# Optimization experiments

Hardware: AMD Instinct MI355X
Metric: run time of the kernel (lower is better)

Reference implementation:

```python
import jax, jax.numpy as jnp
import numpy as np

B, M = 2, 4096
N1, N2, N3 = 16384, 8192, 4096
OFFSET = (0.0, -40.0, -3.0)
LR_VS = (0.4, 0.4, 1.0)
HR1_VS = (0.05, 0.05, 0.1)
HR2_VS = (0.1, 0.1, 0.2)
HR3_VS = (0.2, 0.2, 0.4)
RADIUS = 1.0
NS1, NS2, NS3 = 128, 32, 16
BN_EPS = 1e-3


def _rand_idx(key, n, dims):
    kz, ky, kx = jax.random.split(key, 3)
    z = jax.random.randint(kz, (B, n, 1), 0, dims[0], dtype=jnp.int32)
    y = jax.random.randint(ky, (B, n, 1), 0, dims[1], dtype=jnp.int32)
    x = jax.random.randint(kx, (B, n, 1), 0, dims[2], dtype=jnp.int32)
    return jnp.concatenate([z, y, x], axis=-1)


def setup_inputs() -> dict:
    key = jax.random.key(0)
    ks = jax.random.split(key, 16)
    s = 0.1
    inp = {}
    # voxel indices are (z, y, x) per the original coors layout
    inp["lr_idx"] = _rand_idx(ks[0], M, (5, 200, 176))
    inp["hr1_idx"] = _rand_idx(ks[1], N1, (40, 1600, 1408))
    inp["hr2_idx"] = _rand_idx(ks[2], N2, (20, 800, 704))
    inp["hr3_idx"] = _rand_idx(ks[3], N3, (10, 400, 352))
    inp["lr_feat"] = jax.random.normal(ks[4], (B, M, 64), jnp.float32)
    inp["hr1_feat"] = jax.random.normal(ks[5], (B, N1, 16), jnp.float32)
    inp["hr2_feat"] = jax.random.normal(ks[6], (B, N2, 32), jnp.float32)
    inp["hr3_feat"] = jax.random.normal(ks[7], (B, N3, 64), jnp.float32)
    # Grouper shared-MLP weights (single layer each; +3 channels for use_xyz)
    inp["w14"] = jax.random.normal(ks[8], (19, 32), jnp.float32) * s
    inp["b14"] = jnp.zeros((32,), jnp.float32)
    inp["w24"] = jax.random.normal(ks[9], (35, 32), jnp.float32) * s
    inp["b24"] = jnp.zeros((32,), jnp.float32)
    inp["w34"] = jax.random.normal(ks[10], (67, 32), jnp.float32) * s
    inp["b34"] = jnp.zeros((32,), jnp.float32)
    # conv4_out: 1x1x1 sparse conv == dense matmul per voxel, then BN + ReLU
    inp["w_out"] = jax.random.normal(ks[11], (160, 64), jnp.float32) * s
    inp["bn_gamma"] = jnp.ones((64,), jnp.float32)
    inp["bn_beta"] = jnp.zeros((64,), jnp.float32)
    inp["bn_mean"] = jnp.zeros((64,), jnp.float32)
    inp["bn_var"] = jnp.ones((64,), jnp.float32)
    return inp


def idx_to_xyz(idx, vs):
    # indices are (z,y,x); original does indices[:, [3,2,1]] * voxel_size + offset + 0.5*voxel_size
    vs = jnp.asarray(vs, jnp.float32)
    off = jnp.asarray(OFFSET, jnp.float32)
    return idx[..., ::-1].astype(jnp.float32) * vs + off + 0.5 * vs


def ball_query(lr_xyz, hr_xyz, nsample):
    # first-nsample-within-radius semantics of pointnet2 ball_query
    d2 = jnp.sum((lr_xyz[:, None, :] - hr_xyz[None, :, :]) ** 2, axis=-1)  # [M, N]
    n = hr_xyz.shape[0]
    cand = jnp.where(d2 < RADIUS * RADIUS, jnp.arange(n, dtype=jnp.int32), n)
    neg, _ = jax.lax.top_k(-cand, nsample)  # smallest nsample candidate indices
    idx = -neg
    idx = jnp.where(idx == n, idx[:, :1], idx)  # pad with first valid neighbor
    return jnp.where(idx == n, 0, idx)          # no neighbor at all -> index 0


def group_pool(lr_xyz, hr_xyz, hr_feat, nsample, w, b):
    idx = ball_query(lr_xyz, hr_xyz, nsample)          # [M, ns]
    g_xyz = hr_xyz[idx] - lr_xyz[:, None, :]           # [M, ns, 3] relative coords
    g = jnp.concatenate([g_xyz, hr_feat[idx]], axis=-1)  # [M, ns, 3+C]
    h = jax.nn.relu(jnp.einsum('msc,co->mso', g, w) + b)
    return h.max(axis=1)                                # [M, Cout] max-pool over neighbors


def reference(lr_idx, hr1_idx, hr2_idx, hr3_idx, lr_feat, hr1_feat, hr2_feat, hr3_feat,
              w14, b14, w24, b24, w34, b34, w_out, bn_gamma, bn_beta, bn_mean, bn_var):
    lr_xyz = idx_to_xyz(lr_idx, LR_VS)                  # [B, M, 3]
    f14 = jax.vmap(lambda l, h, f: group_pool(l, h, f, NS1, w14, b14))(lr_xyz, idx_to_xyz(hr1_idx, HR1_VS), hr1_feat)
    f24 = jax.vmap(lambda l, h, f: group_pool(l, h, f, NS2, w24, b24))(lr_xyz, idx_to_xyz(hr2_idx, HR2_VS), hr2_feat)
    f34 = jax.vmap(lambda l, h, f: group_pool(l, h, f, NS3, w34, b34))(lr_xyz, idx_to_xyz(hr3_idx, HR3_VS), hr3_feat)
    cat = jnp.concatenate([lr_feat, f14, f24, f34], axis=-1)  # [B, M, 160] (in-place feature growth)
    y = jnp.einsum('bmc,co->bmo', cat, w_out)
    y = (y - bn_mean) * jax.lax.rsqrt(bn_var + BN_EPS) * bn_gamma + bn_beta
    return jax.nn.relu(y)
```

## Files before the change

### kernel.cpp

```cpp
#include <hip/hip_runtime.h>

#define BM   8192
#define NN1  16384
#define NN2  8192
#define NN3  4096
#define NB   80
#define NBLK 32
#define CHUNK 2048
#define TSZ  768
#define QCAP 512

#define OFF_LRS   0
#define OFF_S1    32768
#define OFF_S2    163840
#define OFF_S3    229376
#define OFF_F1    262144
#define OFF_F2    1310720
#define OFF_F3    1835008
#define OFF_PART  2097152
#define OFF_START 2117632
#define OFF_WP    2118656
#define OFF_SHIFT 2128896
#define WS_FLOATS 2128960


__global__ __launch_bounds__(256) void kprep(
    const int* __restrict__ lr_idx, const int* __restrict__ h1i,
    const int* __restrict__ h2i, const int* __restrict__ h3i,
    const float* __restrict__ f1, const float* __restrict__ f2, const float* __restrict__ f3,
    const float* __restrict__ w14, const float* __restrict__ b14,
    const float* __restrict__ w24, const float* __restrict__ b24,
    const float* __restrict__ w34, const float* __restrict__ b34,
    const float* __restrict__ wout, const float* __restrict__ gam,
    const float* __restrict__ bet, const float* __restrict__ mean,
    const float* __restrict__ var, float* __restrict__ ws)
{
    __shared__ int hist[640];
    int bx = blockIdx.x, tid = threadIdx.x;

    if (bx < NBLK) {
        for (int e = tid; e < 640; e += 256) hist[e] = 0;
        __syncthreads();
        int base_it = bx * CHUNK;
        for (int t = tid; t < CHUNK; t += 256) {
            int e = base_it + t;
            int T, iy; float vsx;
            if (e < 8192)            { T = 6 + (e>>12); iy = lr_idx[e*3+1]; vsx = 0.4f; }
            else { int r = e - 8192;
              if (r < 32768)         { int b = r>>14; T = b;   iy = h1i[r*3+1]; vsx = 0.05f; }
              else { r -= 32768;
                if (r < 16384)       { int b = r>>13; T = 2+b; iy = h2i[r*3+1]; vsx = 0.1f; }
                else { r -= 16384; int b = r>>12; T = 4+b; iy = h3i[r*3+1]; vsx = 0.2f; }
              }
            }
            float y = __fadd_rn(__fadd_rn(__fmul_rn((float)iy, vsx), -40.0f), __fmul_rn(0.5f, vsx));
            int k = min(NB-1, max(0, (int)floorf(y + 40.0f)));
            atomicAdd(&hist[T*80 + k], 1);
        }
        __syncthreads();
        for (int e = tid; e < 640; e += 256)
            reinterpret_cast<int*>(ws)[OFF_PART + bx*640 + e] = hist[e];
        return;
    }

    int e = (bx - NBLK) * 256 + tid;

    if (e < 262144) {
        int o2 = e & 7, jj = e >> 3;
        const float4* fv = reinterpret_cast<const float4*>(f1) + jj*4;
        const float4* w4 = reinterpret_cast<const float4*>(w14);
        float4 acc = reinterpret_cast<const float4*>(b14)[o2];
        float fr[16];
        #pragma unroll
        for (int c4 = 0; c4 < 4; ++c4) {
            float4 f = fv[c4];
            fr[c4*4] = f.x; fr[c4*4+1] = f.y; fr[c4*4+2] = f.z; fr[c4*4+3] = f.w;
        }
        #pragma unroll
        for (int c = 0; c < 16; ++c) {
            float4 w = w4[(3+c)*8 + o2];
            acc.x = fmaf(fr[c], w.x, acc.x); acc.y = fmaf(fr[c], w.y, acc.y);
            acc.z = fmaf(fr[c], w.z, acc.z); acc.w = fmaf(fr[c], w.w, acc.w);
        }
        reinterpret_cast<float4*>(ws + OFF_F1)[jj*8 + o2] = acc;
        return;
    }
    e -= 262144;
    if (e < 131072) {
        int o2 = e & 7, jj = e >> 3;
        const float4* fv = reinterpret_cast<const float4*>(f2) + jj*8;
        const float4* w4 = reinterpret_cast<const float4*>(w24);
        float4 acc = reinterpret_cast<const float4*>(b24)[o2];
        #pragma unroll
        for (int cc = 0; cc < 32; cc += 16) {
            float fr[16];
            #pragma unroll
            for (int c4 = 0; c4 < 4; ++c4) {
                float4 f = fv[cc/4 + c4];
                fr[c4*4] = f.x; fr[c4*4+1] = f.y; fr[c4*4+2] = f.z; fr[c4*4+3] = f.w;
            }
            #pragma unroll
            for (int c = 0; c < 16; ++c) {
                float4 w = w4[(3+cc+c)*8 + o2];
                acc.x = fmaf(fr[c], w.x, acc.x); acc.y = fmaf(fr[c], w.y, acc.y);
                acc.z = fmaf(fr[c], w.z, acc.z); acc.w = fmaf(fr[c], w.w, acc.w);
            }
        }
        reinterpret_cast<float4*>(ws + OFF_F2)[jj*8 + o2] = acc;
        return;
    }
    e -= 131072;
    if (e < 65536) {
        int o2 = e & 7, jj = e >> 3;
        const float4* fv = reinterpret_cast<const float4*>(f3) + jj*16;
        const float4* w4 = reinterpret_cast<const float4*>(w34);
        float4 acc = reinterpret_cast<const float4*>(b34)[o2];
        #pragma unroll
        for (int cc = 0; cc < 64; cc += 16) {
            float fr[16];
            #pragma unroll
            for (int c4 = 0; c4 < 4; ++c4) {
                float4 f = fv[cc/4 + c4];
                fr[c4*4] = f.x; fr[c4*4+1] = f.y; fr[c4*4+2] = f.z; fr[c4*4+3] = f.w;
            }
            #pragma unroll
            for (int c = 0; c < 16; ++c) {
                float4 w = w4[(3+cc+c)*8 + o2];
                acc.x = fmaf(fr[c], w.x, acc.x); acc.y = fmaf(fr[c], w.y, acc.y);
                acc.z = fmaf(fr[c], w.z, acc.z); acc.w = fmaf(fr[c], w.w, acc.w);
            }
        }
        reinterpret_cast<float4*>(ws + OFF_F3)[jj*8 + o2] = acc;
        return;
    }
    e -= 65536;

    if (e < 10240) {
        int o = e & 63;
        float sc = gam[o] * (1.0f / sqrtf(var[o] + 1e-3f));
        ws[OFF_WP + e] = wout[e] * sc;
    } else if (e < 10304) {
        int o = e - 10240;
        float sc = gam[o] * (1.0f / sqrtf(var[o] + 1e-3f));
        ws[OFF_SHIFT + o] = bet[o] - mean[o] * sc;
    }
}

__global__ __launch_bounds__(1024) void ksort(
    const int* __restrict__ lr_idx, const int* __restrict__ h1i,
    const int* __restrict__ h2i, const int* __restrict__ h3i,
    float* __restrict__ ws)
{
    __shared__ int totS[640];
    __shared__ int stt[648];
    __shared__ int cur[640];
    int t = threadIdx.x, bx = blockIdx.x;
    int* wsi = reinterpret_cast<int*>(ws);

    int tot = 0, mypre = 0;
    if (t < 640) {
        #pragma unroll
        for (int b = 0; b < NBLK; ++b) {
            int p = wsi[OFF_PART + b*640 + t];
            tot += p;
            if (b < bx) mypre += p;
        }
        totS[t] = tot;
    }
    __syncthreads();
    int wid = t >> 6, lane = t & 63;
    if (wid < 8) {
        int v = totS[wid*80 + lane];
        #pragma unroll
        for (int s = 1; s < 64; s <<= 1) { int u = __shfl_up(v, s); if (lane >= s) v += u; }
        int base64 = __shfl(v, 63);
        int v2 = (lane < 16) ? totS[wid*80 + 64 + lane] : 0;
        #pragma unroll
        for (int s = 1; s < 16; s <<= 1) { int u = __shfl_up(v2, s); if (lane >= s) v2 += u; }
        if (lane == 0) stt[wid*81] = 0;
        stt[wid*81 + 1 + lane] = v;
        if (lane < 16) stt[wid*81 + 65 + lane] = base64 + v2;
    }
    __syncthreads();
    if (bx == 0 && t < 648) wsi[OFF_START + t] = stt[t];
    if (t < 640) cur[t] = stt[(t/80)*81 + (t%80)] + mypre;
    __syncthreads();

    int base_it = bx * CHUNK;
    for (int tt = t; tt < CHUNK; tt += 1024) {
        int e = base_it + tt;
        int T, w, dst4, r3; const int* ip; float vsx, vsz;
        if (e < 8192) {
            int b = e >> 12; T = 6+b; ip = lr_idx; r3 = e*3; vsx = 0.4f; vsz = 1.0f;
            w = e; dst4 = OFF_LRS/4 + b*4096;
        } else { int r = e - 8192;
          if (r < 32768) { int b = r>>14; T = b;   ip = h1i; r3 = r*3; vsx = 0.05f; vsz = 0.1f; w = r - b*NN1; dst4 = OFF_S1/4 + b*NN1; }
          else { r -= 32768;
            if (r < 16384) { int b = r>>13; T = 2+b; ip = h2i; r3 = r*3; vsx = 0.1f; vsz = 0.2f; w = r - b*NN2; dst4 = OFF_S2/4 + b*NN2; }
            else { r -= 16384; int b = r>>12; T = 4+b; ip = h3i; r3 = r*3; vsx = 0.2f; vsz = 0.4f; w = r - b*NN3; dst4 = OFF_S3/4 + b*NN3; }
          }
        }
        int iz = ip[r3], iy = ip[r3+1], ix = ip[r3+2];
        float4 v;
        v.x = __fadd_rn(__fadd_rn(__fmul_rn((float)ix, vsx),   0.0f), __fmul_rn(0.5f, vsx));
        v.y = __fadd_rn(__fadd_rn(__fmul_rn((float)iy, vsx), -40.0f), __fmul_rn(0.5f, vsx));
        v.z = __fadd_rn(__fadd_rn(__fmul_rn((float)iz, vsz),  -3.0f), __fmul_rn(0.5f, vsz));
        v.w = __int_as_float(w);
        int k = min(NB-1, max(0, (int)floorf(v.y + 40.0f)));
        int pos = atomicAdd(&cur[T*80 + k], 1);
        reinterpret_cast<float4*>(ws)[dst4 + pos] = v;
    }
}

__global__ __launch_bounds__(512) void kmain(
    float* __restrict__ ws, const float* __restrict__ lr_feat,
    const int* __restrict__ h1i, const int* __restrict__ h2i, const int* __restrict__ h3i,
    const float* __restrict__ w14, const float* __restrict__ w24, const float* __restrict__ w34,
    float* __restrict__ out)
{
    __shared__ float4 Sst[TSZ];
    __shared__ float  catS[32][160];
    __shared__ int    accS[32*33];
    __shared__ float  lrS[32*4];
    __shared__ float  wAll[288];
    __shared__ int    cntS[32];
    __shared__ int    porigS[32];
    __shared__ int    queue[QCAP];
    __shared__ int    qn;

    int pg = blockIdx.x;
    int b  = pg >> 7;
    int tid = threadIdx.x, lane = tid & 63, half = lane >> 5, p = lane & 31, wv = tid >> 6;

    if (tid < 96)        wAll[tid] = w14[tid];
    else if (tid < 192)  wAll[tid] = w24[tid-96];
    else if (tid < 288)  wAll[tid] = w34[tid-192];
    for (int e = tid; e < 32*33; e += 512) accS[e] = 0;
    if (tid < 32) {
        float4 l = reinterpret_cast<const float4*>(ws + OFF_LRS)[pg*32 + tid];
        reinterpret_cast<float4*>(lrS)[tid] = l;
        porigS[tid] = __float_as_int(l.w);
        cntS[tid] = 0;
    }
    if (tid == 0) qn = 0;

    float4 lr = reinterpret_cast<const float4*>(ws + OFF_LRS)[pg*32 + p];
    float ymin = lr.y, ymax = lr.y;
    #pragma unroll
    for (int m = 1; m < 32; m <<= 1) {
        ymin = fminf(ymin, __shfl_xor(ymin, m));
        ymax = fmaxf(ymax, __shfl_xor(ymax, m));
    }
    int klo = max(0, (int)floorf(ymin - 1.001f + 40.0f));
    int khi = min(NB-1, (int)floorf(ymax + 1.001f + 40.0f));

    __syncthreads();

    for (int e = tid; e < 2048; e += 512) {
        int i = e >> 6, c = e & 63;
        catS[i][c] = lr_feat[porigS[i]*64 + c];
    }

    #pragma unroll 1
    for (int s = 0; s < 3; ++s) {
        const int* hidx; int soff, Foff, N, wb; float vsx, vsz;
        if (s == 0)      { hidx=h1i; soff=OFF_S1; Foff=OFF_F1; N=NN1; vsx=0.05f; vsz=0.1f; wb=0; }
        else if (s == 1) { hidx=h2i; soff=OFF_S2; Foff=OFF_F2; N=NN2; vsx=0.1f;  vsz=0.2f; wb=96; }
        else             { hidx=h3i; soff=OFF_S3; Foff=OFF_F3; N=NN3; vsx=0.2f;  vsz=0.4f; wb=192; }

        const int* st = reinterpret_cast<const int*>(ws) + OFF_START + (s*2+b)*81;
        int j0 = st[klo], j1 = st[khi+1];
        const float4* S  = reinterpret_cast<const float4*>(ws + soff) + b*N;
        const float* Fb = ws + Foff + (size_t)b*N*32;

        for (int t0 = j0; t0 < j1; t0 += TSZ) {
            int tlen = min(TSZ, j1 - t0);
            __syncthreads();
            for (int e = tid; e < tlen; e += 512) Sst[e] = S[t0 + e];
            __syncthreads();

            int a   = (tlen * wv) >> 3;
            int bnd = (tlen * (wv+1)) >> 3;
            for (int j = a + half; j < bnd; j += 2) {
                float4 q = Sst[j];
                float dx = q.x - lr.x, dy = q.y - lr.y, dz = q.z - lr.z;
                float d2 = __fadd_rn(__fadd_rn(__fmul_rn(dx,dx), __fmul_rn(dy,dy)), __fmul_rn(dz,dz));
                if (d2 < 1.0f) {
                    cntS[p] = 1;
                    int pos = atomicAdd(&qn, 1);
                    if (pos < QCAP) queue[pos] = (j << 5) | p;
                }
            }
            __syncthreads();

            int nh = min(qn, QCAP);
            for (int e = tid; e < nh*32; e += 512) {
                int ent = queue[e >> 5], o = e & 31;
                int jl = ent >> 5, pp = ent & 31;
                float4 q = Sst[jl];
                float dx = q.x - lrS[pp*4], dy = q.y - lrS[pp*4+1], dz = q.z - lrS[pp*4+2];
                int jo = __float_as_int(q.w);
                float h = Fb[(size_t)jo*32 + o] + dx*wAll[wb+o] + dy*wAll[wb+32+o] + dz*wAll[wb+64+o];
                atomicMax(&accS[pp*33 + o], __float_as_int(h));
            }
            __syncthreads();
            if (tid == 0) qn = 0;
        }

        int i0 = b * N * 3;
        int hz = hidx[i0], hy = hidx[i0+1], hx = hidx[i0+2];
        float q0x = __fadd_rn(__fadd_rn(__fmul_rn((float)hx, vsx),   0.0f), __fmul_rn(0.5f, vsx));
        float q0y = __fadd_rn(__fadd_rn(__fmul_rn((float)hy, vsx), -40.0f), __fmul_rn(0.5f, vsx));
        float q0z = __fadd_rn(__fadd_rn(__fmul_rn((float)hz, vsz),  -3.0f), __fmul_rn(0.5f, vsz));

        for (int e = tid; e < 1024; e += 512) {
            int i = e >> 5, o = e & 31;
            float v;
            if (cntS[i]) v = __int_as_float(accS[i*33 + o]);
            else {
                float dx = q0x - lrS[i*4], dy = q0y - lrS[i*4+1], dz = q0z - lrS[i*4+2];
                v = fmaxf(Fb[o] + dx*wAll[wb+o] + dy*wAll[wb+32+o] + dz*wAll[wb+64+o], 0.f);
            }
            catS[i][64 + s*32 + o] = v;
        }
        __syncthreads();
        for (int e = tid; e < 32*33; e += 512) accS[e] = 0;
        if (tid < 32) cntS[tid] = 0;
    }
    __syncthreads();

    float sh = ws[OFF_SHIFT + lane];
    float acc[4] = {sh, sh, sh, sh};
    const float* wp = ws + OFF_WP;
    #pragma unroll 2
    for (int c = 0; c < 160; c += 4) {
        float w0 = wp[(c+0)*64 + lane];
        float w1 = wp[(c+1)*64 + lane];
        float w2 = wp[(c+2)*64 + lane];
        float w3 = wp[(c+3)*64 + lane];
        #pragma unroll
        for (int pt = 0; pt < 4; ++pt) {
            float4 cv = *reinterpret_cast<const float4*>(&catS[wv*4 + pt][c]);
            acc[pt] = fmaf(cv.x, w0, acc[pt]);
            acc[pt] = fmaf(cv.y, w1, acc[pt]);
            acc[pt] = fmaf(cv.z, w2, acc[pt]);
            acc[pt] = fmaf(cv.w, w3, acc[pt]);
        }
    }
    #pragma unroll
    for (int pt = 0; pt < 4; ++pt)
        out[porigS[wv*4 + pt]*64 + lane] = fmaxf(acc[pt], 0.f);
}

extern "C" void kernel_launch(void* const* d_in, const int* in_sizes, int n_in,
                              void* d_out, int out_size, void* d_ws, size_t ws_size,
                              hipStream_t stream) {
    const int*   lr_idx = (const int*)d_in[0];
    const int*   h1i    = (const int*)d_in[1];
    const int*   h2i    = (const int*)d_in[2];
    const int*   h3i    = (const int*)d_in[3];
    const float* lrf    = (const float*)d_in[4];
    const float* f1     = (const float*)d_in[5];
    const float* f2     = (const float*)d_in[6];
    const float* f3     = (const float*)d_in[7];
    const float* w14    = (const float*)d_in[8];
    const float* b14    = (const float*)d_in[9];
    const float* w24    = (const float*)d_in[10];
    const float* b24    = (const float*)d_in[11];
    const float* w34    = (const float*)d_in[12];
    const float* b34    = (const float*)d_in[13];
    const float* wout   = (const float*)d_in[14];
    const float* gam    = (const float*)d_in[15];
    const float* bet    = (const float*)d_in[16];
    const float* mean   = (const float*)d_in[17];
    const float* var    = (const float*)d_in[18];
    float* ws  = (float*)d_ws;
    float* out = (float*)d_out;

    if (ws_size < (size_t)WS_FLOATS * sizeof(float)) return;

    kprep<<<1865, 256, 0, stream>>>(lr_idx, h1i, h2i, h3i, f1, f2, f3,
                                    w14, b14, w24, b24, w34, b34,
                                    wout, gam, bet, mean, var, ws);
    ksort<<<NBLK, 1024, 0, stream>>>(lr_idx, h1i, h2i, h3i, ws);
    kmain<<<256, 512, 0, stream>>>(ws, lrf, h1i, h2i, h3i, w14, w24, w34, out);
}
```

Before: 140.8 us.

## Fuse histogram and counting-sort kernels by redundantly computing full histogram per block

Merges the prep and sort kernels into one launch. Each of the 32 sort blocks now builds the full histogram over all 65536 points, plus its own exclusive prefix, instead of exchanging per-block partial histograms through global memory. This removes one kernel launch and the global partial-histogram round trip. In exchange each block does 32x redundant index reads and shared atomics, and the feature-projection blocks now use 1024 threads.

```diff
diff --git a/kernel.cpp b/kernel.cpp
--- a/kernel.cpp
+++ b/kernel.cpp
@@ -17,14 +17,29 @@
 #define OFF_F1    262144
 #define OFF_F2    1310720
 #define OFF_F3    1835008
-#define OFF_PART  2097152
-#define OFF_START 2117632
-#define OFF_WP    2118656
-#define OFF_SHIFT 2128896
-#define WS_FLOATS 2128960
-
-
-__global__ __launch_bounds__(256) void kprep(
+#define OFF_START 2097152
+#define OFF_WP    2098176
+#define OFF_SHIFT 2108416
+#define WS_FLOATS 2108480
+
+
+__device__ __forceinline__ void classify(
+    int e, const int* lr_idx, const int* h1i, const int* h2i, const int* h3i,
+    int& T, const int*& ip, int& r3, float& vsx, float& vsz, int& w, int& dst4)
+{
+    if (e < 8192) {
+        int b = e >> 12; T = 6+b; ip = lr_idx; r3 = e*3; vsx = 0.4f; vsz = 1.0f;
+        w = e; dst4 = OFF_LRS/4 + b*4096;
+    } else { int r = e - 8192;
+      if (r < 32768) { int b = r>>14; T = b;   ip = h1i; r3 = r*3; vsx = 0.05f; vsz = 0.1f; w = r - b*NN1; dst4 = OFF_S1/4 + b*NN1; }
+      else { r -= 32768;
+        if (r < 16384) { int b = r>>13; T = 2+b; ip = h2i; r3 = r*3; vsx = 0.1f; vsz = 0.2f; w = r - b*NN2; dst4 = OFF_S2/4 + b*NN2; }
+        else { r -= 16384; int b = r>>12; T = 4+b; ip = h3i; r3 = r*3; vsx = 0.2f; vsz = 0.4f; w = r - b*NN3; dst4 = OFF_S3/4 + b*NN3; }
+      }
+    }
+}
+
+__global__ __launch_bounds__(1024) void kall(
     const int* __restrict__ lr_idx, const int* __restrict__ h1i,
     const int* __restrict__ h2i, const int* __restrict__ h3i,
     const float* __restrict__ f1, const float* __restrict__ f2, const float* __restrict__ f3,
@@ -35,35 +50,61 @@
     const float* __restrict__ bet, const float* __restrict__ mean,
     const float* __restrict__ var, float* __restrict__ ws)
 {
-    __shared__ int hist[640];
+    __shared__ int tot[640];
+    __shared__ int pre[640];
+    __shared__ int stt[648];
+    __shared__ int cur[640];
     int bx = blockIdx.x, tid = threadIdx.x;
 
     if (bx < NBLK) {
-        for (int e = tid; e < 640; e += 256) hist[e] = 0;
-        __syncthreads();
-        int base_it = bx * CHUNK;
-        for (int t = tid; t < CHUNK; t += 256) {
-            int e = base_it + t;
-            int T, iy; float vsx;
-            if (e < 8192)            { T = 6 + (e>>12); iy = lr_idx[e*3+1]; vsx = 0.4f; }
-            else { int r = e - 8192;
-              if (r < 32768)         { int b = r>>14; T = b;   iy = h1i[r*3+1]; vsx = 0.05f; }
-              else { r -= 32768;
-                if (r < 16384)       { int b = r>>13; T = 2+b; iy = h2i[r*3+1]; vsx = 0.1f; }
-                else { r -= 16384; int b = r>>12; T = 4+b; iy = h3i[r*3+1]; vsx = 0.2f; }
-              }
-            }
+        if (tid < 640) { tot[tid] = 0; pre[tid] = 0; }
+        __syncthreads();
+        int mybase = bx * CHUNK;
+        for (int e = tid; e < 65536; e += 1024) {
+            int T, r3, w, dst4; const int* ip; float vsx, vsz;
+            classify(e, lr_idx, h1i, h2i, h3i, T, ip, r3, vsx, vsz, w, dst4);
+            int iy = ip[r3 + 1];
             float y = __fadd_rn(__fadd_rn(__fmul_rn((float)iy, vsx), -40.0f), __fmul_rn(0.5f, vsx));
             int k = min(NB-1, max(0, (int)floorf(y + 40.0f)));
-            atomicAdd(&hist[T*80 + k], 1);
-        }
-        __syncthreads();
-        for (int e = tid; e < 640; e += 256)
-            reinterpret_cast<int*>(ws)[OFF_PART + bx*640 + e] = hist[e];
+            atomicAdd(&tot[T*80 + k], 1);
+            if (e < mybase) atomicAdd(&pre[T*80 + k], 1);
+        }
+        __syncthreads();
+        int wid = tid >> 6, lane = tid & 63;
+        if (wid < 8) {
+            int v = tot[wid*80 + lane];
+            #pragma unroll
+            for (int s = 1; s < 64; s <<= 1) { int u = __shfl_up(v, s); if (lane >= s) v += u; }
+            int base64 = __shfl(v, 63);
+            int v2 = (lane < 16) ? tot[wid*80 + 64 + lane] : 0;
+            #pragma unroll
+            for (int s = 1; s < 16; s <<= 1) { int u = __shfl_up(v2, s); if (lane >= s) v2 += u; }
+            if (lane == 0) stt[wid*81] = 0;
+            stt[wid*81 + 1 + lane] = v;
+            if (lane < 16) stt[wid*81 + 65 + lane] = base64 + v2;
+        }
+        __syncthreads();
+        if (bx == 0 && tid < 648) reinterpret_cast<int*>(ws)[OFF_START + tid] = stt[tid];
+        if (tid < 640) cur[tid] = stt[(tid/80)*81 + (tid%80)] + pre[tid];
+        __syncthreads();
+        for (int t = tid; t < CHUNK; t += 1024) {
+            int e = mybase + t;
+            int T, r3, w, dst4; const int* ip; float vsx, vsz;
+            classify(e, lr_idx, h1i, h2i, h3i, T, ip, r3, vsx, vsz, w, dst4);
+            int iz = ip[r3], iy = ip[r3+1], ix = ip[r3+2];
+            float4 v;
+            v.x = __fadd_rn(__fadd_rn(__fmul_rn((float)ix, vsx),   0.0f), __fmul_rn(0.5f, vsx));
+            v.y = __fadd_rn(__fadd_rn(__fmul_rn((float)iy, vsx), -40.0f), __fmul_rn(0.5f, vsx));
+            v.z = __fadd_rn(__fadd_rn(__fmul_rn((float)iz, vsz),  -3.0f), __fmul_rn(0.5f, vsz));
+            v.w = __int_as_float(w);
+            int k = min(NB-1, max(0, (int)floorf(v.y + 40.0f)));
+            int pos = atomicAdd(&cur[T*80 + k], 1);
+            reinterpret_cast<float4*>(ws)[dst4 + pos] = v;
+        }
         return;
     }
 
-    int e = (bx - NBLK) * 256 + tid;
+    int e = (bx - NBLK) * 1024 + tid;
 
     if (e < 262144) {
         int o2 = e & 7, jj = e >> 3;
@@ -143,72 +184,6 @@
         int o = e - 10240;
         float sc = gam[o] * (1.0f / sqrtf(var[o] + 1e-3f));
         ws[OFF_SHIFT + o] = bet[o] - mean[o] * sc;
-    }
-}
-
-__global__ __launch_bounds__(1024) void ksort(
-    const int* __restrict__ lr_idx, const int* __restrict__ h1i,
-    const int* __restrict__ h2i, const int* __restrict__ h3i,
-    float* __restrict__ ws)
-{
-    __shared__ int totS[640];
-    __shared__ int stt[648];
-    __shared__ int cur[640];
-    int t = threadIdx.x, bx = blockIdx.x;
-    int* wsi = reinterpret_cast<int*>(ws);
-
-    int tot = 0, mypre = 0;
-    if (t < 640) {
-        #pragma unroll
-        for (int b = 0; b < NBLK; ++b) {
-            int p = wsi[OFF_PART + b*640 + t];
-            tot += p;
-            if (b < bx) mypre += p;
-        }
-        totS[t] = tot;
-    }
-    __syncthreads();
-    int wid = t >> 6, lane = t & 63;
-    if (wid < 8) {
-        int v = totS[wid*80 + lane];
-        #pragma unroll
-        for (int s = 1; s < 64; s <<= 1) { int u = __shfl_up(v, s); if (lane >= s) v += u; }
-        int base64 = __shfl(v, 63);
-        int v2 = (lane < 16) ? totS[wid*80 + 64 + lane] : 0;
-        #pragma unroll
-        for (int s = 1; s < 16; s <<= 1) { int u = __shfl_up(v2, s); if (lane >= s) v2 += u; }
-        if (lane == 0) stt[wid*81] = 0;
-        stt[wid*81 + 1 + lane] = v;
-        if (lane < 16) stt[wid*81 + 65 + lane] = base64 + v2;
-    }
-    __syncthreads();
-    if (bx == 0 && t < 648) wsi[OFF_START + t] = stt[t];
-    if (t < 640) cur[t] = stt[(t/80)*81 + (t%80)] + mypre;
-    __syncthreads();
-
-    int base_it = bx * CHUNK;
-    for (int tt = t; tt < CHUNK; tt += 1024) {
-        int e = base_it + tt;
-        int T, w, dst4, r3; const int* ip; float vsx, vsz;
-        if (e < 8192) {
-            int b = e >> 12; T = 6+b; ip = lr_idx; r3 = e*3; vsx = 0.4f; vsz = 1.0f;
-            w = e; dst4 = OFF_LRS/4 + b*4096;
-        } else { int r = e - 8192;
-          if (r < 32768) { int b = r>>14; T = b;   ip = h1i; r3 = r*3; vsx = 0.05f; vsz = 0.1f; w = r - b*NN1; dst4 = OFF_S1/4 + b*NN1; }
-          else { r -= 32768;
-            if (r < 16384) { int b = r>>13; T = 2+b; ip = h2i; r3 = r*3; vsx = 0.1f; vsz = 0.2f; w = r - b*NN2; dst4 = OFF_S2/4 + b*NN2; }
-            else { r -= 16384; int b = r>>12; T = 4+b; ip = h3i; r3 = r*3; vsx = 0.2f; vsz = 0.4f; w = r - b*NN3; dst4 = OFF_S3/4 + b*NN3; }
-          }
-        }
-        int iz = ip[r3], iy = ip[r3+1], ix = ip[r3+2];
-        float4 v;
-        v.x = __fadd_rn(__fadd_rn(__fmul_rn((float)ix, vsx),   0.0f), __fmul_rn(0.5f, vsx));
-        v.y = __fadd_rn(__fadd_rn(__fmul_rn((float)iy, vsx), -40.0f), __fmul_rn(0.5f, vsx));
-        v.z = __fadd_rn(__fadd_rn(__fmul_rn((float)iz, vsz),  -3.0f), __fmul_rn(0.5f, vsz));
-        v.w = __int_as_float(w);
-        int k = min(NB-1, max(0, (int)floorf(v.y + 40.0f)));
-        int pos = atomicAdd(&cur[T*80 + k], 1);
-        reinterpret_cast<float4*>(ws)[dst4 + pos] = v;
     }
 }
 
@@ -379,9 +354,8 @@
 
     if (ws_size < (size_t)WS_FLOATS * sizeof(float)) return;
 
-    kprep<<<1865, 256, 0, stream>>>(lr_idx, h1i, h2i, h3i, f1, f2, f3,
-                                    w14, b14, w24, b24, w34, b34,
-                                    wout, gam, bet, mean, var, ws);
-    ksort<<<NBLK, 1024, 0, stream>>>(lr_idx, h1i, h2i, h3i, ws);
+    kall<<<491, 1024, 0, stream>>>(lr_idx, h1i, h2i, h3i, f1, f2, f3,
+                                   w14, b14, w24, b24, w34, b34,
+                                   wout, gam, bet, mean, var, ws);
     kmain<<<256, 512, 0, stream>>>(ws, lrf, h1i, h2i, h3i, w14, w24, w34, out);
 }
```

Result: slower. 158.8 us (+12.8%).
